# Kernel tuning notes

Hardware: AMD Instinct MI355X
Metric: run time of the kernel (lower is better)

The kernel has to match this reference:

```python
import jax, jax.numpy as jnp
import numpy as np

EPS = 1e-7          # self.eps[float32]
MIN_NORM = 1e-15
PROJ_EPS = 4e-3     # PoincareBall proj epsilon (float32)
FD_R = 2.0          # args.r
FD_T = 1.0          # args.t
DIS_CLIP = 40.0     # args.dis_mx_clip
ATT_BETA = 0.2      # args.att_beta
# curvature c = 1.0 (self.cur = [1.0, ...]); sqrt_c = 1 so it is folded out below.

def _norm(x):
    return jnp.maximum(jnp.linalg.norm(x, axis=-1, keepdims=True), MIN_NORM)

def expmap0(u):
    n = _norm(u)
    return jnp.tanh(n) * u / n

def proj(x):
    n = _norm(x)
    maxnorm = 1.0 - PROJ_EPS
    return jnp.where(n > maxnorm, x / n * maxnorm, x)

def proj_tan0_exp(u):
    return proj(expmap0(u))

def artanh(x):
    x = jnp.clip(x, -1.0 + EPS, 1.0 - EPS)
    return 0.5 * (jnp.log1p(x) - jnp.log1p(-x))

def mobius_add(x, y):
    x2 = jnp.sum(x * x, -1, keepdims=True)
    y2 = jnp.sum(y * y, -1, keepdims=True)
    xy = jnp.sum(x * y, -1, keepdims=True)
    num = (1.0 + 2.0 * xy + y2) * x + (1.0 - x2) * y
    den = 1.0 + 2.0 * xy + x2 * y2
    return num / jnp.maximum(den, MIN_NORM)

def sqdist(p, q):
    d = 2.0 * artanh(jnp.linalg.norm(mobius_add(-p, q), axis=-1))
    return d * d

def to_klein(x):
    return 2.0 * x / (1.0 + jnp.sum(x * x, -1, keepdims=True))

def lorentz_factor(x):
    return 1.0 / jnp.sqrt(jnp.maximum(1.0 - jnp.sum(x * x, -1), EPS))

def klein_to(x):
    return x / (1.0 + jnp.sqrt(jnp.maximum(1.0 - jnp.sum(x * x, -1, keepdims=True), EPS)))

N_ENTITY, N_REL, DIM = 200000, 32, 64
B, H, M = 1024, 2, 32

def setup_inputs() -> dict:
    key = jax.random.key(0)
    ks = jax.random.split(key, 9)
    return {
        'users': jax.random.randint(ks[0], (B,), 0, 10000),
        'items': jax.random.randint(ks[1], (B,), 0, N_ENTITY),
        'labels': jax.random.randint(ks[2], (B,), 0, 2),
        'mem_h': jax.random.randint(ks[3], (H, B, M), 0, N_ENTITY),
        'mem_r': jax.random.randint(ks[4], (H, B, M), 0, N_REL),
        'mem_t': jax.random.randint(ks[5], (H, B, M), 0, N_ENTITY),
        'entity_emb': 0.05 * jax.random.normal(ks[6], (N_ENTITY, DIM), dtype=jnp.float32),
        'rela_plus_emb': 0.05 * jax.random.normal(ks[7], (N_REL, DIM), dtype=jnp.float32),
        'relation_emb': 0.1 * jax.random.normal(ks[8], (N_REL, DIM * DIM), dtype=jnp.float32),
    }

def reference(users, items, labels, mem_h, mem_r, mem_t,
              entity_emb, rela_plus_emb, relation_emb):
    d = entity_emb.shape[-1]
    item = entity_emb[items]                                  # [B, d]
    h = entity_emb[mem_h]                                     # [H, B, M, d]
    t = entity_emb[mem_t]                                     # [H, B, M, d]
    R = relation_emb[mem_r].reshape(*mem_r.shape, d, d) / 10.0  # [H, B, M, d, d]
    # relation-transform of heads, mapped to the Poincare ball (dropout=eval/identity)
    Rh = proj_tan0_exp(jnp.einsum('hbmij,hbmj->hbmi', R, h))  # [H, B, M, d]
    hyp_item = proj(proj_tan0_exp(item))                      # [B, d] (res = proj(hyp_item))
    dist2 = sqdist(Rh, hyp_item[None, :, None, :])            # [H, B, M]
    att = jnp.exp(-ATT_BETA * dist2 - 0.05)
    kle_t = to_klein(proj_tan0_exp(t))                        # [H, B, M, d]
    p1 = lorentz_factor(kle_t) * att                          # [H, B, M]
    w1 = p1 / jnp.maximum(jnp.sum(p1, -1, keepdims=True), EPS)
    kle_o = jnp.einsum('hbm,hbmd->bhd', w1, kle_t)            # [B, H, d]
    # hop aggregation (one_like_bahop is all-ones)
    p2 = lorentz_factor(kle_o)                                # [B, H]
    w2 = p2 / jnp.maximum(jnp.sum(p2, -1, keepdims=True), EPS)
    o = jnp.einsum('bh,bhd->bd', w2, kle_o)                   # [B, d]
    hyp_o = proj(klein_to(o))
    d2 = sqdist(hyp_o, proj_tan0_exp(item))                   # [B]
    scores = 1.0 / (jnp.exp(jnp.minimum(d2 - FD_R, DIS_CLIP) / FD_T) + 1.0)
    return scores
```

## Files before the change

kernel.cpp:

```cpp
#include <hip/hip_runtime.h>
#include <hip/hip_bf16.h>

#define DIMV 64
#define PWB  32
#define RELS 32
#define RPITCH 17

typedef float f32x4 __attribute__((ext_vector_type(4)));

static constexpr float F_EPS  = 1e-7f;
static constexpr float F_MINN = 1e-15f;
static constexpr float F_MAXN = 1.0f - 4e-3f;

__device__ __forceinline__ float frcp(float x) { return __builtin_amdgcn_rcpf(x); }
__device__ __forceinline__ float frsq(float x) { return __builtin_amdgcn_rsqf(x); }
__device__ __forceinline__ float tanh_fast(float x) {
    float e = __expf(2.0f * x);
    return 1.0f - 2.0f * frcp(e + 1.0f);
}

__device__ __forceinline__ float wave_sum1(float v) {
#pragma unroll
    for (int off = 32; off > 0; off >>= 1) v += __shfl_xor(v, off, 64);
    return v;
}
__device__ __forceinline__ void wave_sum2(float& a, float& b) {
#pragma unroll
    for (int off = 32; off > 0; off >>= 1) {
        a += __shfl_xor(a, off, 64);
        b += __shfl_xor(b, off, 64);
    }
}
__device__ __forceinline__ void wave_sum3(float& a, float& b, float& c) {
#pragma unroll
    for (int off = 32; off > 0; off >>= 1) {
        a += __shfl_xor(a, off, 64);
        b += __shfl_xor(b, off, 64);
        c += __shfl_xor(c, off, 64);
    }
}

__global__ __launch_bounds__(256) void k_prep(
        const int*   __restrict__ mr,
        const int*   __restrict__ items,
        const float* __restrict__ ent,
        int*         __restrict__ cursor,
        int*         __restrict__ bins,
        float*       __restrict__ qbuf,
        float*       __restrict__ y2buf,
        int n, int B, int cap)
{
    __shared__ int lcnt[RELS], lbase[RELS];
    const int tid = threadIdx.x;
    if (tid < RELS) lcnt[tid] = 0;
    __syncthreads();

    const int i = blockIdx.x * 256 + tid;
    int r = 0, rnk = 0;
    const bool valid = (i < n);
    if (valid) {
        r = mr[i];
        rnk = atomicAdd(&lcnt[r], 1);
    }
    __syncthreads();
    if (tid < RELS) lbase[tid] = lcnt[tid] ? atomicAdd(&cursor[tid], lcnt[tid]) : 0;
    __syncthreads();
    if (valid) {
        int pos = lbase[r] + rnk;
        if (pos < cap) bins[(long)r * cap + pos] = i;
    }

    const int wave = tid >> 6, lane = tid & 63;
    const int b = blockIdx.x * 4 + wave;
    if (b >= B) return;
    const int it = items[b];
    const float iv = ent[(long)it * DIMV + lane];
    float n2 = wave_sum1(iv * iv);
    float nn = fmaxf(sqrtf(n2), F_MINN);
    float te = tanh_fast(nn);
    float s  = (te > F_MAXN) ? F_MAXN * frcp(te) : 1.0f;
    qbuf[(long)b * DIMV + lane] = iv * (te * frcp(nn)) * s;
    if (lane == 0) { float qn = te * s; y2buf[b] = qn * qn; }
}

template<int MM, int BB>
__global__ __launch_bounds__(256) void k_main(
        const int*   __restrict__ mem_h,
        const int*   __restrict__ mem_t,
        const float* __restrict__ ent,
        const float* __restrict__ rel,
        const int*   __restrict__ cursor,
        const int*   __restrict__ bins,
        const float* __restrict__ qbuf,
        const float* __restrict__ y2buf,
        float*       __restrict__ acc,
        int M, int B, int cap)
{
    const int r      = blockIdx.y;
    const int cnt    = min(cursor[r], cap);
    const int cstart = blockIdx.x * PWB;
    if (cstart >= cnt) return;

    __shared__ f32x4 Rl[DIMV * RPITCH];
    {
        const int t  = threadIdx.x;
        const int i  = t >> 2, qr = t & 3;
        const f32x4* Rg = (const f32x4*)(rel + (long)r * (DIMV * DIMV));
#pragma unroll
        for (int s = 0; s < 4; ++s)
            Rl[i * RPITCH + qr * 4 + s] = Rg[i * 16 + qr * 4 + s];
    }
    __syncthreads();

    const int lane   = threadIdx.x & 63;
    const int wave   = threadIdx.x >> 6;
    const int wstart = cstart + wave * 8;
    const int wcnt   = min(cnt - wstart, 8);
    if (wcnt <= 0) return;
    const int* mybin = bins + (long)r * cap;

    for (int p = 0; p < 2; ++p) {
        const int np = min(wcnt - p * 4, 4);
        if (np <= 0) break;

        const float* hpI[4];
        int   hbI[4];
        float tvI[4], qI[4], y2I[4];
#pragma unroll
        for (int nn = 0; nn < 4; ++nn) {
            const int kk  = wstart + p * 4 + ((nn < np) ? nn : 0);
            const int t   = __builtin_amdgcn_readfirstlane(mybin[kk]);
            const int ih  = __builtin_amdgcn_readfirstlane(mem_h[t]);
            const int itt = __builtin_amdgcn_readfirstlane(mem_t[t]);
            const int hb  = MM ? (t / MM) : (int)((unsigned)t / (unsigned)M);
            const int b   = BB ? (hb & (BB - 1)) : (hb % B);
            hbI[nn] = hb;
            hpI[nn] = ent + (long)ih * DIMV;
            tvI[nn] = ent[(long)itt * DIMV + lane];
            qI[nn]  = qbuf[(long)b * DIMV + lane];
            y2I[nn] = y2buf[b];
        }

        float u[4][4] = {};
#pragma unroll
        for (int j = 0; j < 16; ++j) {
            const f32x4 rv = Rl[lane * RPITCH + j];
#pragma unroll
            for (int nn = 0; nn < 4; ++nn) {
                u[nn][0] = fmaf(rv.x, hpI[nn][4 * j + 0], u[nn][0]);
                u[nn][1] = fmaf(rv.y, hpI[nn][4 * j + 1], u[nn][1]);
                u[nn][2] = fmaf(rv.z, hpI[nn][4 * j + 2], u[nn][2]);
                u[nn][3] = fmaf(rv.w, hpI[nn][4 * j + 3], u[nn][3]);
            }
        }

#pragma unroll
        for (int nn = 0; nn < 4; ++nn) {
            const float un = ((u[nn][0] + u[nn][1]) + (u[nn][2] + u[nn][3])) * 0.1f;
            float uu = un * un, uq = un * qI[nn], tt = tvI[nn] * tvI[nn];
            wave_sum3(uu, uq, tt);

            float nu = fmaxf(sqrtf(uu), F_MINN);
            float te = tanh_fast(nu);
            float sc = (te > F_MAXN) ? F_MAXN * frcp(te) : 1.0f;
            float pn = te * sc;
            float x2 = pn * pn;
            float xy = -(pn * frcp(nu)) * uq;
            float y2 = y2I[nn];

            float A_  = 1.0f + 2.0f * xy + y2;
            float B_  = 1.0f - x2;
            float nm2 = fmaxf(A_ * A_ * x2 + B_ * B_ * y2 + 2.0f * A_ * B_ * xy, 0.0f);
            float den = fmaxf(1.0f + 2.0f * xy + x2 * y2, 1e-15f);
            float v   = fminf(sqrtf(nm2) * frcp(den), 1.0f - F_EPS);
            float dd  = __logf((1.0f + v) * frcp(1.0f - v));
            float att = __expf(fmaf(-0.2f, dd * dd, -0.05f));

            float nt  = fmaxf(sqrtf(tt), F_MINN);
            float tte = tanh_fast(nt);
            float ts  = (tte > F_MAXN) ? F_MAXN * frcp(tte) : 1.0f;
            float ptn = tte * ts;
            float a2  = ptn * ptn;
            float i1a = frcp(1.0f + a2);
            float kn2 = 4.0f * a2 * i1a * i1a;
            float lf  = frsq(fmaxf(1.0f - kn2, F_EPS));
            float p1  = lf * att;
            float kfc = 2.0f * ptn * frcp(nt) * i1a;

            if (nn < np) {
                float* slot = acc + (long)hbI[nn] * 65;
                atomicAdd(slot + lane, p1 * kfc * tvI[nn]);
                if (lane == 0) atomicAdd(slot + 64, p1);
            }
        }
    }
}

__global__ __launch_bounds__(256) void k_fin(
        const float* __restrict__ acc,
        const float* __restrict__ qbuf,
        const float* __restrict__ y2buf,
        float*       __restrict__ out,
        int B)
{
    const int wave = threadIdx.x >> 6, lane = threadIdx.x & 63;
    const int b = blockIdx.x * 4 + wave;
    if (b >= B) return;

    const float q  = qbuf[(long)b * DIMV + lane];
    const float y2 = y2buf[b];

    const float* s0 = acc + (long)b * 65;
    const float* s1 = acc + (long)(B + b) * 65;
    float k0 = s0[lane] * frcp(fmaxf(s0[64], F_EPS));
    float k1 = s1[lane] * frcp(fmaxf(s1[64], F_EPS));

    float n0 = k0 * k0, n1 = k1 * k1;
    wave_sum2(n0, n1);
    float p20 = frsq(fmaxf(1.0f - n0, F_EPS));
    float p21 = frsq(fmaxf(1.0f - n1, F_EPS));
    float o   = (p20 * k0 + p21 * k1) * frcp(fmaxf(p20 + p21, F_EPS));

    float oo = o * o, oq = o * q;
    wave_sum2(oo, oq);
    float kd    = 1.0f + sqrtf(fmaxf(1.0f - oo, F_EPS));
    float invkd = frcp(kd);
    float ko2   = oo * invkd * invkd;
    float nk    = fmaxf(sqrtf(ko2), F_MINN);
    float ps    = (nk > F_MAXN) ? F_MAXN * frcp(nk) : 1.0f;
    float x2    = (nk * ps) * (nk * ps);
    float xy    = -(ps * invkd) * oq;

    float A_  = 1.0f + 2.0f * xy + y2;
    float B_  = 1.0f - x2;
    float nm2 = fmaxf(A_ * A_ * x2 + B_ * B_ * y2 + 2.0f * A_ * B_ * xy, 0.0f);
    float den = fmaxf(1.0f + 2.0f * xy + x2 * y2, 1e-15f);
    float v   = fminf(sqrtf(nm2) * frcp(den), 1.0f - F_EPS);
    float dd  = __logf((1.0f + v) * frcp(1.0f - v));
    float d2  = dd * dd;

    float scr = frcp(__expf(fminf(d2 - 2.0f, 40.0f)) + 1.0f);
    if (lane == 0) out[b] = scr;
}

extern "C" void kernel_launch(void* const* d_in, const int* in_sizes, int n_in,
                              void* d_out, int out_size, void* d_ws, size_t ws_size,
                              hipStream_t stream) {
    const int*   items = (const int*)d_in[1];
    const int*   mh    = (const int*)d_in[3];
    const int*   mr    = (const int*)d_in[4];
    const int*   mt    = (const int*)d_in[5];
    const float* ent   = (const float*)d_in[6];
    const float* rel   = (const float*)d_in[8];
    float* out = (float*)d_out;

    const int B = in_sizes[1];
    const int n = in_sizes[3];
    const int M = n / (2 * B);
    const bool fastpath = (M == 32 && B == 1024 && n == 65536);
    const int cap = fastpath ? 2560 : n;

    int*   cursor = (int*)d_ws;
    float* acc    = (float*)(cursor + 32);
    size_t zero_bytes = 32 * sizeof(int) + (size_t)2 * B * 65 * sizeof(float);
    int*   bins   = (int*)((char*)d_ws + zero_bytes);
    float* qbuf   = (float*)(bins + (size_t)RELS * cap);
    float* y2buf  = qbuf + (size_t)B * DIMV;

    hipMemsetAsync(d_ws, 0, zero_bytes, stream);

    {
        int gp = (n + 255) / 256;
        int gq = (B + 3) / 4;
        int g  = gp > gq ? gp : gq;
        k_prep<<<dim3(g), dim3(256), 0, stream>>>(mr, items, ent, cursor, bins,
                                                  qbuf, y2buf, n, B, cap);
    }

    dim3 gmain((cap + PWB - 1) / PWB, RELS);
    if (fastpath)
        k_main<32, 1024><<<gmain, dim3(256), 0, stream>>>(
            mh, mt, ent, rel, cursor, bins, qbuf, y2buf, acc, M, B, cap);
    else
        k_main<0, 0><<<gmain, dim3(256), 0, stream>>>(
            mh, mt, ent, rel, cursor, bins, qbuf, y2buf, acc, M, B, cap);

    k_fin<<<dim3((B + 3) / 4), dim3(256), 0, stream>>>(acc, qbuf, y2buf, out, B);
}
```

Before: 159.0 us.

## Replace atomic scatter with per-item scalar buffer and per-batch gather reduction

The main kernel no longer scatters weighted tail vectors with atomics. It stages the relation-transformed heads in shared memory, computes the attention and Klein scalars for 8 items per wave in parallel (8 lanes per item, shorter shuffle tree), and writes only a (p1, kfc) pair per memory slot. A new per-batch kernel then gathers the tail embeddings in original order, reduces them without atomics, and fuses the final hop aggregation and scoring. This drops the large accumulator memset and the atomic contention, at the cost of reading the tail embeddings a second time.

```diff
diff --git a/kernel.cpp b/kernel.cpp
--- a/kernel.cpp
+++ b/kernel.cpp
@@ -4,7 +4,7 @@
 #define DIMV 64
 #define PWB  32
 #define RELS 32
-#define RPITCH 17
+#define UPITCH 68
 
 typedef float f32x4 __attribute__((ext_vector_type(4)));
 
@@ -29,14 +29,6 @@
     for (int off = 32; off > 0; off >>= 1) {
         a += __shfl_xor(a, off, 64);
         b += __shfl_xor(b, off, 64);
-    }
-}
-__device__ __forceinline__ void wave_sum3(float& a, float& b, float& c) {
-#pragma unroll
-    for (int off = 32; off > 0; off >>= 1) {
-        a += __shfl_xor(a, off, 64);
-        b += __shfl_xor(b, off, 64);
-        c += __shfl_xor(c, off, 64);
     }
 }
 
@@ -84,7 +76,7 @@
 }
 
 template<int MM, int BB>
-__global__ __launch_bounds__(256) void k_main(
+__global__ __launch_bounds__(256) void k_A(
         const int*   __restrict__ mem_h,
         const int*   __restrict__ mem_t,
         const float* __restrict__ ent,
@@ -93,7 +85,7 @@
         const int*   __restrict__ bins,
         const float* __restrict__ qbuf,
         const float* __restrict__ y2buf,
-        float*       __restrict__ acc,
+        float2*      __restrict__ pkbuf,
         int M, int B, int cap)
 {
     const int r      = blockIdx.y;
@@ -101,14 +93,16 @@
     const int cstart = blockIdx.x * PWB;
     if (cstart >= cnt) return;
 
-    __shared__ f32x4 Rl[DIMV * RPITCH];
+    __shared__ float Rl[DIMV * UPITCH];
+    __shared__ float Ut[4][8 * UPITCH];
     {
-        const int t  = threadIdx.x;
-        const int i  = t >> 2, qr = t & 3;
-        const f32x4* Rg = (const f32x4*)(rel + (long)r * (DIMV * DIMV));
-#pragma unroll
-        for (int s = 0; s < 4; ++s)
-            Rl[i * RPITCH + qr * 4 + s] = Rg[i * 16 + qr * 4 + s];
+        const f32x4* Rg  = (const f32x4*)(rel + (long)r * (DIMV * DIMV));
+        f32x4*       Rl4 = (f32x4*)Rl;
+#pragma unroll
+        for (int s = 0; s < 4; ++s) {
+            const int idx = threadIdx.x * 4 + s;
+            Rl4[(idx >> 4) * 17 + (idx & 15)] = Rg[idx];
+        }
     }
     __syncthreads();
 
@@ -118,33 +112,24 @@
     const int wcnt   = min(cnt - wstart, 8);
     if (wcnt <= 0) return;
     const int* mybin = bins + (long)r * cap;
+    float* myU = &Ut[wave][0];
+    const f32x4* Rl4 = (const f32x4*)Rl;
 
     for (int p = 0; p < 2; ++p) {
         const int np = min(wcnt - p * 4, 4);
         if (np <= 0) break;
-
         const float* hpI[4];
-        int   hbI[4];
-        float tvI[4], qI[4], y2I[4];
 #pragma unroll
         for (int nn = 0; nn < 4; ++nn) {
-            const int kk  = wstart + p * 4 + ((nn < np) ? nn : 0);
-            const int t   = __builtin_amdgcn_readfirstlane(mybin[kk]);
-            const int ih  = __builtin_amdgcn_readfirstlane(mem_h[t]);
-            const int itt = __builtin_amdgcn_readfirstlane(mem_t[t]);
-            const int hb  = MM ? (t / MM) : (int)((unsigned)t / (unsigned)M);
-            const int b   = BB ? (hb & (BB - 1)) : (hb % B);
-            hbI[nn] = hb;
+            const int kk = wstart + p * 4 + ((nn < np) ? nn : 0);
+            const int t  = __builtin_amdgcn_readfirstlane(mybin[kk]);
+            const int ih = __builtin_amdgcn_readfirstlane(mem_h[t]);
             hpI[nn] = ent + (long)ih * DIMV;
-            tvI[nn] = ent[(long)itt * DIMV + lane];
-            qI[nn]  = qbuf[(long)b * DIMV + lane];
-            y2I[nn] = y2buf[b];
         }
-
         float u[4][4] = {};
 #pragma unroll
         for (int j = 0; j < 16; ++j) {
-            const f32x4 rv = Rl[lane * RPITCH + j];
+            const f32x4 rv = Rl4[lane * 17 + j];
 #pragma unroll
             for (int nn = 0; nn < 4; ++nn) {
                 u[nn][0] = fmaf(rv.x, hpI[nn][4 * j + 0], u[nn][0]);
@@ -153,83 +138,47 @@
                 u[nn][3] = fmaf(rv.w, hpI[nn][4 * j + 3], u[nn][3]);
             }
         }
-
-#pragma unroll
-        for (int nn = 0; nn < 4; ++nn) {
-            const float un = ((u[nn][0] + u[nn][1]) + (u[nn][2] + u[nn][3])) * 0.1f;
-            float uu = un * un, uq = un * qI[nn], tt = tvI[nn] * tvI[nn];
-            wave_sum3(uu, uq, tt);
-
-            float nu = fmaxf(sqrtf(uu), F_MINN);
-            float te = tanh_fast(nu);
-            float sc = (te > F_MAXN) ? F_MAXN * frcp(te) : 1.0f;
-            float pn = te * sc;
-            float x2 = pn * pn;
-            float xy = -(pn * frcp(nu)) * uq;
-            float y2 = y2I[nn];
-
-            float A_  = 1.0f + 2.0f * xy + y2;
-            float B_  = 1.0f - x2;
-            float nm2 = fmaxf(A_ * A_ * x2 + B_ * B_ * y2 + 2.0f * A_ * B_ * xy, 0.0f);
-            float den = fmaxf(1.0f + 2.0f * xy + x2 * y2, 1e-15f);
-            float v   = fminf(sqrtf(nm2) * frcp(den), 1.0f - F_EPS);
-            float dd  = __logf((1.0f + v) * frcp(1.0f - v));
-            float att = __expf(fmaf(-0.2f, dd * dd, -0.05f));
-
-            float nt  = fmaxf(sqrtf(tt), F_MINN);
-            float tte = tanh_fast(nt);
-            float ts  = (tte > F_MAXN) ? F_MAXN * frcp(tte) : 1.0f;
-            float ptn = tte * ts;
-            float a2  = ptn * ptn;
-            float i1a = frcp(1.0f + a2);
-            float kn2 = 4.0f * a2 * i1a * i1a;
-            float lf  = frsq(fmaxf(1.0f - kn2, F_EPS));
-            float p1  = lf * att;
-            float kfc = 2.0f * ptn * frcp(nt) * i1a;
-
-            if (nn < np) {
-                float* slot = acc + (long)hbI[nn] * 65;
-                atomicAdd(slot + lane, p1 * kfc * tvI[nn]);
-                if (lane == 0) atomicAdd(slot + 64, p1);
-            }
-        }
-    }
-}
-
-__global__ __launch_bounds__(256) void k_fin(
-        const float* __restrict__ acc,
-        const float* __restrict__ qbuf,
-        const float* __restrict__ y2buf,
-        float*       __restrict__ out,
-        int B)
-{
-    const int wave = threadIdx.x >> 6, lane = threadIdx.x & 63;
-    const int b = blockIdx.x * 4 + wave;
-    if (b >= B) return;
-
-    const float q  = qbuf[(long)b * DIMV + lane];
+#pragma unroll
+        for (int nn = 0; nn < 4; ++nn)
+            myU[(p * 4 + nn) * UPITCH + lane] =
+                ((u[nn][0] + u[nn][1]) + (u[nn][2] + u[nn][3])) * 0.1f;
+    }
+
+    const int tk  = lane & 7;
+    const int oct = lane >> 3;
+    const int kk  = wstart + ((tk < wcnt) ? tk : 0);
+    const int t   = mybin[kk];
+    const int itt = mem_t[t];
+    const int hb  = MM ? (t / MM) : (int)((unsigned)t / (unsigned)M);
+    const int b   = BB ? (hb & (BB - 1)) : (hb % B);
     const float y2 = y2buf[b];
 
-    const float* s0 = acc + (long)b * 65;
-    const float* s1 = acc + (long)(B + b) * 65;
-    float k0 = s0[lane] * frcp(fmaxf(s0[64], F_EPS));
-    float k1 = s1[lane] * frcp(fmaxf(s1[64], F_EPS));
-
-    float n0 = k0 * k0, n1 = k1 * k1;
-    wave_sum2(n0, n1);
-    float p20 = frsq(fmaxf(1.0f - n0, F_EPS));
-    float p21 = frsq(fmaxf(1.0f - n1, F_EPS));
-    float o   = (p20 * k0 + p21 * k1) * frcp(fmaxf(p20 + p21, F_EPS));
-
-    float oo = o * o, oq = o * q;
-    wave_sum2(oo, oq);
-    float kd    = 1.0f + sqrtf(fmaxf(1.0f - oo, F_EPS));
-    float invkd = frcp(kd);
-    float ko2   = oo * invkd * invkd;
-    float nk    = fmaxf(sqrtf(ko2), F_MINN);
-    float ps    = (nk > F_MAXN) ? F_MAXN * frcp(nk) : 1.0f;
-    float x2    = (nk * ps) * (nk * ps);
-    float xy    = -(ps * invkd) * oq;
+    const float4* qr = (const float4*)(qbuf + (long)b  * DIMV) + oct * 2;
+    const float4* tr = (const float4*)(ent  + (long)itt * DIMV) + oct * 2;
+    const float4 q0 = qr[0], q1 = qr[1];
+    const float4 t0 = tr[0], t1 = tr[1];
+    const f32x4* Up = (const f32x4*)&myU[tk * UPITCH + oct * 8];
+    const f32x4 uA = Up[0], uB = Up[1];
+
+    float uu = uA.x*uA.x + uA.y*uA.y + uA.z*uA.z + uA.w*uA.w
+             + uB.x*uB.x + uB.y*uB.y + uB.z*uB.z + uB.w*uB.w;
+    float uq = uA.x*q0.x + uA.y*q0.y + uA.z*q0.z + uA.w*q0.w
+             + uB.x*q1.x + uB.y*q1.y + uB.z*q1.z + uB.w*q1.w;
+    float tt = t0.x*t0.x + t0.y*t0.y + t0.z*t0.z + t0.w*t0.w
+             + t1.x*t1.x + t1.y*t1.y + t1.z*t1.z + t1.w*t1.w;
+#pragma unroll
+    for (int off = 8; off < 64; off <<= 1) {
+        uu += __shfl_xor(uu, off, 64);
+        uq += __shfl_xor(uq, off, 64);
+        tt += __shfl_xor(tt, off, 64);
+    }
+
+    float nu = fmaxf(sqrtf(uu), F_MINN);
+    float te = tanh_fast(nu);
+    float sc = (te > F_MAXN) ? F_MAXN * frcp(te) : 1.0f;
+    float pn = te * sc;
+    float x2 = pn * pn;
+    float xy = -(pn * frcp(nu)) * uq;
 
     float A_  = 1.0f + 2.0f * xy + y2;
     float B_  = 1.0f - x2;
@@ -237,10 +186,90 @@
     float den = fmaxf(1.0f + 2.0f * xy + x2 * y2, 1e-15f);
     float v   = fminf(sqrtf(nm2) * frcp(den), 1.0f - F_EPS);
     float dd  = __logf((1.0f + v) * frcp(1.0f - v));
-    float d2  = dd * dd;
-
-    float scr = frcp(__expf(fminf(d2 - 2.0f, 40.0f)) + 1.0f);
-    if (lane == 0) out[b] = scr;
+    float att = __expf(fmaf(-0.2f, dd * dd, -0.05f));
+
+    float nt  = fmaxf(sqrtf(tt), F_MINN);
+    float tte = tanh_fast(nt);
+    float ts  = (tte > F_MAXN) ? F_MAXN * frcp(tte) : 1.0f;
+    float ptn = tte * ts;
+    float a2  = ptn * ptn;
+    float i1a = frcp(1.0f + a2);
+    float kn2 = 4.0f * a2 * i1a * i1a;
+    float lf  = frsq(fmaxf(1.0f - kn2, F_EPS));
+    float p1  = lf * att;
+    float kfc = 2.0f * ptn * frcp(nt) * i1a;
+
+    if (oct == 0 && tk < wcnt) pkbuf[t] = make_float2(p1, kfc);
+}
+
+__global__ __launch_bounds__(256) void k_B(
+        const int*    __restrict__ mem_t,
+        const float*  __restrict__ ent,
+        const float2* __restrict__ pkbuf,
+        const float*  __restrict__ qbuf,
+        const float*  __restrict__ y2buf,
+        float*        __restrict__ out,
+        int B, int M)
+{
+    const int b    = blockIdx.x;
+    const int wave = threadIdx.x >> 6;
+    const int lane = threadIdx.x & 63;
+    const int h    = wave >> 1;
+    const int mhalf = M >> 1;
+    const int mst  = (wave & 1) * mhalf;
+
+    float accA = 0.0f, accS = 0.0f;
+    const long ibase = ((long)h * B + b) * M + mst;
+
+#pragma unroll 4
+    for (int k = 0; k < mhalf; ++k) {
+        const long t  = ibase + k;
+        const int itt = __builtin_amdgcn_readfirstlane(mem_t[t]);
+        const float2 pk = pkbuf[t];
+        const float  tv = ent[(long)itt * DIMV + lane];
+        accS += pk.x;
+        accA = fmaf(pk.x * pk.y, tv, accA);
+    }
+
+    __shared__ float A_l[4][DIMV];
+    __shared__ float S_l[4];
+    A_l[wave][lane] = accA;
+    if (lane == 0) S_l[wave] = accS;
+    __syncthreads();
+
+    if (wave == 0) {
+        const float q  = qbuf[(long)b * DIMV + lane];
+        const float y2 = y2buf[b];
+
+        float k0 = (A_l[0][lane] + A_l[1][lane]) * frcp(fmaxf(S_l[0] + S_l[1], F_EPS));
+        float k1 = (A_l[2][lane] + A_l[3][lane]) * frcp(fmaxf(S_l[2] + S_l[3], F_EPS));
+        float n0 = k0 * k0, n1 = k1 * k1;
+        wave_sum2(n0, n1);
+        float p20 = frsq(fmaxf(1.0f - n0, F_EPS));
+        float p21 = frsq(fmaxf(1.0f - n1, F_EPS));
+        float o   = (p20 * k0 + p21 * k1) * frcp(fmaxf(p20 + p21, F_EPS));
+
+        float oo = o * o, oq = o * q;
+        wave_sum2(oo, oq);
+        float kd    = 1.0f + sqrtf(fmaxf(1.0f - oo, F_EPS));
+        float invkd = frcp(kd);
+        float ko2   = oo * invkd * invkd;
+        float nk    = fmaxf(sqrtf(ko2), F_MINN);
+        float ps    = (nk > F_MAXN) ? F_MAXN * frcp(nk) : 1.0f;
+        float x2    = (nk * ps) * (nk * ps);
+        float xy    = -(ps * invkd) * oq;
+
+        float A_  = 1.0f + 2.0f * xy + y2;
+        float B_  = 1.0f - x2;
+        float nm2 = fmaxf(A_ * A_ * x2 + B_ * B_ * y2 + 2.0f * A_ * B_ * xy, 0.0f);
+        float den = fmaxf(1.0f + 2.0f * xy + x2 * y2, 1e-15f);
+        float v   = fminf(sqrtf(nm2) * frcp(den), 1.0f - F_EPS);
+        float dd  = __logf((1.0f + v) * frcp(1.0f - v));
+        float d2  = dd * dd;
+
+        float scr = frcp(__expf(fminf(d2 - 2.0f, 40.0f)) + 1.0f);
+        if (lane == 0) out[b] = scr;
+    }
 }
 
 extern "C" void kernel_launch(void* const* d_in, const int* in_sizes, int n_in,
@@ -260,14 +289,13 @@
     const bool fastpath = (M == 32 && B == 1024 && n == 65536);
     const int cap = fastpath ? 2560 : n;
 
-    int*   cursor = (int*)d_ws;
-    float* acc    = (float*)(cursor + 32);
-    size_t zero_bytes = 32 * sizeof(int) + (size_t)2 * B * 65 * sizeof(float);
-    int*   bins   = (int*)((char*)d_ws + zero_bytes);
-    float* qbuf   = (float*)(bins + (size_t)RELS * cap);
-    float* y2buf  = qbuf + (size_t)B * DIMV;
-
-    hipMemsetAsync(d_ws, 0, zero_bytes, stream);
+    int*    cursor = (int*)d_ws;
+    int*    bins   = cursor + 32;
+    float*  qbuf   = (float*)(bins + (size_t)RELS * cap);
+    float*  y2buf  = qbuf + (size_t)B * DIMV;
+    float2* pkbuf  = (float2*)(y2buf + B);
+
+    hipMemsetAsync(cursor, 0, 32 * sizeof(int), stream);
 
     {
         int gp = (n + 255) / 256;
@@ -277,13 +305,13 @@
                                                   qbuf, y2buf, n, B, cap);
     }
 
-    dim3 gmain((cap + PWB - 1) / PWB, RELS);
+    dim3 gA((cap + PWB - 1) / PWB, RELS);
     if (fastpath)
-        k_main<32, 1024><<<gmain, dim3(256), 0, stream>>>(
-            mh, mt, ent, rel, cursor, bins, qbuf, y2buf, acc, M, B, cap);
+        k_A<32, 1024><<<gA, dim3(256), 0, stream>>>(
+            mh, mt, ent, rel, cursor, bins, qbuf, y2buf, pkbuf, M, B, cap);
     else
-        k_main<0, 0><<<gmain, dim3(256), 0, stream>>>(
-            mh, mt, ent, rel, cursor, bins, qbuf, y2buf, acc, M, B, cap);
-
-    k_fin<<<dim3((B + 3) / 4), dim3(256), 0, stream>>>(acc, qbuf, y2buf, out, B);
-}
+        k_A<0, 0><<<gA, dim3(256), 0, stream>>>(
+            mh, mt, ent, rel, cursor, bins, qbuf, y2buf, pkbuf, M, B, cap);
+
+    k_B<<<dim3(B), dim3(256), 0, stream>>>(mt, ent, pkbuf, qbuf, y2buf, out, B, M);
+}
```

Measured after the change: 135.1 us. -15.1%, faster.
